# Kernel tuning notes

Hardware: AMD Instinct MI355X
Metric: run time of the kernel (lower is better)

## Reference

```python
import jax, jax.numpy as jnp
import numpy as np

N_NODES = 50000
N_EDGES = 800000
NODE_DIM = 128
EDGE_DIM = 64
HID = 2 * NODE_DIM + EDGE_DIM  # 320


def setup_inputs() -> dict:
    key = jax.random.key(0)
    k1, k2, k3, k4 = jax.random.split(key, 4)
    x = jax.random.normal(k1, (N_NODES, NODE_DIM), dtype=jnp.float32)
    edge_index = jax.random.randint(k2, (2, N_EDGES), 0, N_NODES, dtype=jnp.int32)
    edge_ft = jax.random.normal(k3, (N_EDGES, EDGE_DIM), dtype=jnp.float32)
    kw1, kw2 = jax.random.split(k4)
    scale = 1.0 / np.sqrt(HID)
    W_val = jax.random.uniform(kw1, (NODE_DIM, HID), jnp.float32, -scale, scale)
    b_val = jnp.zeros((NODE_DIM,), jnp.float32)
    W_mul = jax.random.uniform(kw2, (NODE_DIM, HID), jnp.float32, -scale, scale)
    b_mul = jnp.zeros((NODE_DIM,), jnp.float32)
    return {"x": x, "edge_index": edge_index, "edge_ft": edge_ft,
            "W_val": W_val, "b_val": b_val, "W_mul": W_mul, "b_mul": b_mul}


def reference(x, edge_index, edge_ft, W_val, b_val, W_mul, b_mul):
    sender, receiver = edge_index[0], edge_index[1]
    # gather + concat: [E, 2*node_dim + edge_dim]
    c = jnp.concatenate([x[sender], x[receiver], edge_ft], axis=1)
    vals = jax.nn.softplus(c @ W_val.T + b_val)
    gate = jax.nn.sigmoid(c @ W_mul.T + b_mul)
    msg = vals * gate  # [E, node_dim]
    # scatter-sum by receiver into [N, node_dim]
    return jax.ops.segment_sum(msg, receiver, num_segments=x.shape[0])
```

## Files before the change

### kernel.cpp

```cpp
#include <hip/hip_runtime.h>

#define E_EDGES   800000
#define NN_NODES  50000
#define NODE_DIM  128
#define EDGE_DIM  64
#define KDIM      320
#define BM        64
#define BN        64
#define SA        72
#define SM        129
#define SX        136
#define THREADS   512
#define W4UNITS   20480
#define NSCAN     98

typedef _Float16 half8 __attribute__((ext_vector_type(8)));
typedef float    f32x4 __attribute__((ext_vector_type(4)));

__device__ __forceinline__ unsigned short f2h(float f) {
    _Float16 h = (_Float16)f;
    return __builtin_bit_cast(unsigned short, h);
}
__device__ __forceinline__ float h2f(unsigned short u) {
    return (float)__builtin_bit_cast(_Float16, u);
}

__global__ void prep(const float* __restrict__ wv,
                     const float* __restrict__ wm,
                     const int* __restrict__ ei,
                     unsigned short* __restrict__ Wc,
                     unsigned* __restrict__ cnt) {
    int i = blockIdx.x * blockDim.x + threadIdx.x;
    if (i < W4UNITS) {
        const int n4h = (NODE_DIM * KDIM) / 4;
        const float* src = (i < n4h) ? wv : wm;
        int j = (i < n4h) ? i : i - n4h;
        float4 f = ((const float4*)src)[j];
        ushort4 o;
        o.x = f2h(f.x); o.y = f2h(f.y); o.z = f2h(f.z); o.w = f2h(f.w);
        ((ushort4*)Wc)[i] = o;
    } else {
        int e = i - W4UNITS;
        if (e < E_EDGES) atomicAdd(&cnt[ei[E_EDGES + e]], 1u);
    }
}

__global__ void scan1(const unsigned* __restrict__ cnt,
                      unsigned* __restrict__ offs,
                      unsigned* __restrict__ bsum) {
    __shared__ unsigned s[512];
    int tid = threadIdx.x;
    int i = blockIdx.x * 512 + tid;
    unsigned v = (i < NN_NODES) ? cnt[i] : 0u;
    s[tid] = v; __syncthreads();
    for (int off = 1; off < 512; off <<= 1) {
        unsigned t = (tid >= off) ? s[tid - off] : 0u;
        __syncthreads();
        s[tid] += t;
        __syncthreads();
    }
    if (i < NN_NODES) offs[i] = s[tid] - v;
    if (tid == 511) bsum[blockIdx.x] = s[511];
}

__global__ void scan2(unsigned* __restrict__ bsum) {
    __shared__ unsigned s[128];
    int tid = threadIdx.x;
    unsigned v = (tid < NSCAN) ? bsum[tid] : 0u;
    s[tid] = v; __syncthreads();
    for (int off = 1; off < 128; off <<= 1) {
        unsigned t = (tid >= off) ? s[tid - off] : 0u;
        __syncthreads();
        s[tid] += t;
        __syncthreads();
    }
    if (tid < NSCAN) bsum[tid] = s[tid] - v;
}

__global__ void scatter_k(const int* __restrict__ ei,
                          unsigned* __restrict__ offs,
                          const unsigned* __restrict__ bsum,
                          unsigned* __restrict__ perm) {
    int e = blockIdx.x * blockDim.x + threadIdx.x;
    if (e >= E_EDGES) return;
    int r = ei[E_EDGES + e];
    unsigned p = atomicAdd(&offs[r], 1u) + bsum[r >> 9];
    perm[p] = (unsigned)e;
}

__global__ void __launch_bounds__(THREADS, 4)
pcompute(const float* __restrict__ x,
         const unsigned short* __restrict__ Wc,
         const float* __restrict__ bval,
         const float* __restrict__ bmul,
         unsigned short* __restrict__ Ph)
{
    __shared__ unsigned short Xs[BN * SX];
    const int tid  = threadIdx.x;
    const int n0   = blockIdx.x * BN;
    const int lane = tid & 63;
    const int wid  = tid >> 6;
    const int wm   = wid & 1;
    const int wn   = wid >> 1;
    const int q    = lane >> 4;
    const int l16  = lane & 15;

#pragma unroll
    for (int i = 0; i < 2; ++i) {
        int u = tid + i * THREADS;
        int row = u >> 4, seg = u & 15;
        int node = n0 + row;
        if (node >= NN_NODES) node = NN_NODES - 1;
        const float* s = x + (size_t)node * NODE_DIM + seg * 8;
        float4 f0 = ((const float4*)s)[0];
        float4 f1 = ((const float4*)s)[1];
        uint4 v;
        v.x = (unsigned)f2h(f0.x) | ((unsigned)f2h(f0.y) << 16);
        v.y = (unsigned)f2h(f0.z) | ((unsigned)f2h(f0.w) << 16);
        v.z = (unsigned)f2h(f1.x) | ((unsigned)f2h(f1.y) << 16);
        v.w = (unsigned)f2h(f1.z) | ((unsigned)f2h(f1.w) << 16);
        *(uint4*)(&Xs[row * SX + seg * 8]) = v;
    }
    __syncthreads();

#pragma unroll
    for (int nhalf = 0; nhalf < 2; ++nhalf) {
        f32x4 acc[2][4];
        const f32x4 zero4 = {0.f, 0.f, 0.f, 0.f};
#pragma unroll
        for (int mt = 0; mt < 2; ++mt)
#pragma unroll
            for (int nt = 0; nt < 4; ++nt) acc[mt][nt] = zero4;

#pragma unroll
        for (int ks = 0; ks < 4; ++ks) {
            half8 a[2], b[4];
#pragma unroll
            for (int mt = 0; mt < 2; ++mt)
                a[mt] = *(const half8*)(&Xs[(wm * 32 + mt * 16 + l16) * SX + ks * 32 + q * 8]);
#pragma unroll
            for (int nt = 0; nt < 4; ++nt)
                b[nt] = *(const half8*)(Wc + (size_t)(wn * 64 + nt * 16 + l16) * KDIM
                                           + nhalf * 128 + ks * 32 + q * 8);
#pragma unroll
            for (int mt = 0; mt < 2; ++mt)
#pragma unroll
                for (int nt = 0; nt < 4; ++nt)
                    acc[mt][nt] = __builtin_amdgcn_mfma_f32_16x16x32_f16(
                        a[mt], b[nt], acc[mt][nt], 0, 0, 0);
        }

#pragma unroll
        for (int mt = 0; mt < 2; ++mt) {
#pragma unroll
            for (int nt = 0; nt < 4; ++nt) {
                int j  = wn * 64 + nt * 16 + l16;
                int c  = j & 127;
                int vg = j >> 7;
                float bb = 0.f;
                if (nhalf == 0) bb = vg ? bmul[c] : bval[c];
#pragma unroll
                for (int r = 0; r < 4; ++r) {
                    int node = n0 + wm * 32 + mt * 16 + q * 4 + r;
                    if (node < NN_NODES)
                        Ph[(size_t)node * 512 + nhalf * 256 + c * 2 + vg] =
                            f2h(acc[mt][nt][r] + bb);
                }
            }
        }
    }
}

__global__ void __launch_bounds__(THREADS, 4)
cgc_sorted(const unsigned short* __restrict__ Ph,
           const int* __restrict__ ei,
           const float* __restrict__ ef,
           const unsigned short* __restrict__ Wc,
           const unsigned* __restrict__ perm,
           float* __restrict__ out)
{
    __shared__ float msgBuf[BM * SM];
    __shared__ int  eIds[BM];
    __shared__ int  sIdx[BM];
    __shared__ int  rIdx[BM];
    __shared__ int  runStart[BM + 1];
    __shared__ int  slotRecv[BM];
    __shared__ int  nslotsS;

    unsigned short* As = (unsigned short*)msgBuf;

    const int tid  = threadIdx.x;
    const int e0   = blockIdx.x * BM;
    const int lane = tid & 63;
    const int wid  = tid >> 6;
    const int wm   = wid & 1;
    const int wn   = wid >> 1;
    const int q    = lane >> 4;
    const int l16  = lane & 15;

    if (tid < BM) {
        int e = (int)perm[e0 + tid];
        eIds[tid] = e;
        int sN = ei[e];
        int rN = ei[E_EDGES + e];
        sIdx[tid] = sN;
        rIdx[tid] = rN;
        int prev = __shfl_up(rN, 1);
        int flag = (tid == 0) || (prev != rN);
        unsigned long long m = __ballot(flag);
        int slot = __popcll(m & (((unsigned long long)2 << tid) - 1)) - 1;
        if (flag) { runStart[slot] = tid; slotRecv[slot] = rN; }
        if (tid == BM - 1) {
            int ns = (int)__popcll(m);
            nslotsS = ns;
            runStart[ns] = BM;
        }
    }
    __syncthreads();

    {
        int row = tid >> 3, seg = tid & 7;
        const float* s = ef + (size_t)eIds[row] * EDGE_DIM + seg * 8;
        float4 f0 = ((const float4*)s)[0];
        float4 f1 = ((const float4*)s)[1];
        uint4 v;
        v.x = (unsigned)f2h(f0.x) | ((unsigned)f2h(f0.y) << 16);
        v.y = (unsigned)f2h(f0.z) | ((unsigned)f2h(f0.w) << 16);
        v.z = (unsigned)f2h(f1.x) | ((unsigned)f2h(f1.y) << 16);
        v.w = (unsigned)f2h(f1.z) | ((unsigned)f2h(f1.w) << 16);
        *(uint4*)(&As[row * SA + seg * 8]) = v;
    }

    const int nb0 = wn * 32;
    const int nbase[4] = { nb0, nb0 + 16, 128 + nb0, 128 + nb0 + 16 };
    half8 b[2][4];
#pragma unroll
    for (int ks = 0; ks < 2; ++ks)
#pragma unroll
        for (int nt = 0; nt < 4; ++nt)
            b[ks][nt] = *(const half8*)(Wc + (size_t)(nbase[nt] + l16) * KDIM
                                           + 256 + ks * 32 + q * 8);

    f32x4 acc[2][4];
    const f32x4 zero4 = {0.f, 0.f, 0.f, 0.f};
#pragma unroll
    for (int mt = 0; mt < 2; ++mt)
#pragma unroll
        for (int nt = 0; nt < 4; ++nt) acc[mt][nt] = zero4;

    __syncthreads();

#pragma unroll
    for (int ks = 0; ks < 2; ++ks) {
        half8 a[2];
#pragma unroll
        for (int mt = 0; mt < 2; ++mt)
            a[mt] = *(const half8*)(&As[(wm * 32 + mt * 16 + l16) * SA + ks * 32 + q * 8]);
#pragma unroll
        for (int mt = 0; mt < 2; ++mt)
#pragma unroll
            for (int nt = 0; nt < 4; ++nt)
                acc[mt][nt] = __builtin_amdgcn_mfma_f32_16x16x32_f16(
                    a[mt], b[ks][nt], acc[mt][nt], 0, 0, 0);
    }

    __syncthreads();

#pragma unroll
    for (int mt = 0; mt < 2; ++mt) {
#pragma unroll
        for (int r = 0; r < 4; ++r) {
            int row = wm * 32 + mt * 16 + q * 4 + r;
            int sN = sIdx[row];
            int rN = rIdx[row];
            const unsigned* pS = (const unsigned*)(Ph + (size_t)sN * 512);
            const unsigned* pR = (const unsigned*)(Ph + (size_t)rN * 512 + 256);
#pragma unroll
            for (int ct = 0; ct < 2; ++ct) {
                int c = wn * 32 + ct * 16 + l16;
                unsigned us = pS[c];
                unsigned ur = pR[c];
                float v = acc[mt][ct][r]     + h2f((unsigned short)(us & 0xffff))
                                             + h2f((unsigned short)(ur & 0xffff));
                float g = acc[mt][ct + 2][r] + h2f((unsigned short)(us >> 16))
                                             + h2f((unsigned short)(ur >> 16));
                float sp  = fmaxf(v, 0.f) + __logf(1.f + __expf(-fabsf(v)));
                float sig = __builtin_amdgcn_rcpf(1.f + __expf(-g));
                msgBuf[row * SM + c] = sp * sig;
            }
        }
    }
    __syncthreads();

    const int nslots = nslotsS;
    for (int idx = tid; idx < nslots * NODE_DIM; idx += THREADS) {
        int s = idx >> 7, c = idx & 127;
        int rs = runStart[s], re = runStart[s + 1];
        float sum = 0.f;
        for (int row = rs; row < re; ++row) sum += msgBuf[row * SM + c];
        atomicAdd(out + (size_t)slotRecv[s] * NODE_DIM + c, sum);
    }
}

__global__ void __launch_bounds__(THREADS, 4)
cgc_atomic(const unsigned short* __restrict__ Ph,
           const int* __restrict__ ei,
           const float* __restrict__ ef,
           const unsigned short* __restrict__ Wc,
           float* __restrict__ out)
{
    __shared__ unsigned short As[BM * SA];
    __shared__ int sIdx[BM];
    __shared__ int rIdx[BM];

    const int tid  = threadIdx.x;
    const int e0   = blockIdx.x * BM;
    const int lane = tid & 63;
    const int wid  = tid >> 6;
    const int wm   = wid & 1;
    const int wn   = wid >> 1;
    const int q    = lane >> 4;
    const int l16  = lane & 15;

    if (tid < BM) {
        sIdx[tid] = ei[e0 + tid];
        rIdx[tid] = ei[E_EDGES + e0 + tid];
    }
    {
        int row = tid >> 3, seg = tid & 7;
        const float* s = ef + (size_t)(e0 + row) * EDGE_DIM + seg * 8;
        float4 f0 = ((const float4*)s)[0];
        float4 f1 = ((const float4*)s)[1];
        uint4 v;
        v.x = (unsigned)f2h(f0.x) | ((unsigned)f2h(f0.y) << 16);
        v.y = (unsigned)f2h(f0.z) | ((unsigned)f2h(f0.w) << 16);
        v.z = (unsigned)f2h(f1.x) | ((unsigned)f2h(f1.y) << 16);
        v.w = (unsigned)f2h(f1.z) | ((unsigned)f2h(f1.w) << 16);
        *(uint4*)(&As[row * SA + seg * 8]) = v;
    }
    const int nb0 = wn * 32;
    const int nbase[4] = { nb0, nb0 + 16, 128 + nb0, 128 + nb0 + 16 };
    half8 b[2][4];
#pragma unroll
    for (int ks = 0; ks < 2; ++ks)
#pragma unroll
        for (int nt = 0; nt < 4; ++nt)
            b[ks][nt] = *(const half8*)(Wc + (size_t)(nbase[nt] + l16) * KDIM
                                           + 256 + ks * 32 + q * 8);
    f32x4 acc[2][4];
    const f32x4 zero4 = {0.f, 0.f, 0.f, 0.f};
#pragma unroll
    for (int mt = 0; mt < 2; ++mt)
#pragma unroll
        for (int nt = 0; nt < 4; ++nt) acc[mt][nt] = zero4;
    __syncthreads();
#pragma unroll
    for (int ks = 0; ks < 2; ++ks) {
        half8 a[2];
#pragma unroll
        for (int mt = 0; mt < 2; ++mt)
            a[mt] = *(const half8*)(&As[(wm * 32 + mt * 16 + l16) * SA + ks * 32 + q * 8]);
#pragma unroll
        for (int mt = 0; mt < 2; ++mt)
#pragma unroll
            for (int nt = 0; nt < 4; ++nt)
                acc[mt][nt] = __builtin_amdgcn_mfma_f32_16x16x32_f16(
                    a[mt], b[ks][nt], acc[mt][nt], 0, 0, 0);
    }
#pragma unroll
    for (int mt = 0; mt < 2; ++mt) {
#pragma unroll
        for (int r = 0; r < 4; ++r) {
            int row = wm * 32 + mt * 16 + q * 4 + r;
            int sN = sIdx[row];
            int rN = rIdx[row];
            const unsigned* pS = (const unsigned*)(Ph + (size_t)sN * 512);
            const unsigned* pR = (const unsigned*)(Ph + (size_t)rN * 512 + 256);
#pragma unroll
            for (int ct = 0; ct < 2; ++ct) {
                int c = wn * 32 + ct * 16 + l16;
                unsigned us = pS[c];
                unsigned ur = pR[c];
                float v = acc[mt][ct][r]     + h2f((unsigned short)(us & 0xffff))
                                             + h2f((unsigned short)(ur & 0xffff));
                float g = acc[mt][ct + 2][r] + h2f((unsigned short)(us >> 16))
                                             + h2f((unsigned short)(ur >> 16));
                float sp  = fmaxf(v, 0.f) + __logf(1.f + __expf(-fabsf(v)));
                float sig = __builtin_amdgcn_rcpf(1.f + __expf(-g));
                atomicAdd(out + (size_t)rN * NODE_DIM + c, sp * sig);
            }
        }
    }
}


extern "C" void kernel_launch(void* const* d_in, const int* in_sizes, int n_in,
                              void* d_out, int out_size, void* d_ws, size_t ws_size,
                              hipStream_t stream) {
    const float* x  = (const float*)d_in[0];
    const int*   ei = (const int*)d_in[1];
    const float* ef = (const float*)d_in[2];
    const float* Wv = (const float*)d_in[3];
    const float* bv = (const float*)d_in[4];
    const float* Wm = (const float*)d_in[5];
    const float* bm = (const float*)d_in[6];
    float* out = (float*)d_out;

    const size_t oWc   = 0;
    const size_t oPh   = 262144;
    const size_t oCnt  = oPh  + 51200000;
    const size_t oOffs = oCnt + 200704;
    const size_t oBsum = oOffs + 200704;
    const size_t oPerm = oBsum + 512;
    const size_t need_sorted = oPerm + (size_t)E_EDGES * 4;

    unsigned short* Wc = (unsigned short*)((char*)d_ws + oWc);
    unsigned short* Ph = (unsigned short*)((char*)d_ws + oPh);

    hipMemsetAsync(d_out, 0, (size_t)NN_NODES * NODE_DIM * sizeof(float), stream);

    if (ws_size >= need_sorted) {
        unsigned* cnt  = (unsigned*)((char*)d_ws + oCnt);
        unsigned* offs = (unsigned*)((char*)d_ws + oOffs);
        unsigned* bsum = (unsigned*)((char*)d_ws + oBsum);
        unsigned* perm = (unsigned*)((char*)d_ws + oPerm);

        hipMemsetAsync(cnt, 0, NN_NODES * sizeof(unsigned), stream);

        const int totalPrep = W4UNITS + E_EDGES;
        prep<<<(totalPrep + 255) / 256, 256, 0, stream>>>(Wv, Wm, ei, Wc, cnt);
        scan1<<<NSCAN, 512, 0, stream>>>(cnt, offs, bsum);
        scan2<<<1, 128, 0, stream>>>(bsum);
        scatter_k<<<(E_EDGES + 255) / 256, 256, 0, stream>>>(ei, offs, bsum, perm);

        pcompute<<<(NN_NODES + BN - 1) / BN, THREADS, 0, stream>>>(x, Wc, bv, bm, Ph);
        cgc_sorted<<<E_EDGES / BM, THREADS, 0, stream>>>(Ph, ei, ef, Wc, perm, out);
    } else {
        prep<<<(W4UNITS + 255) / 256, 256, 0, stream>>>(Wv, Wm, ei, Wc,
                                                        (unsigned*)((char*)d_ws + oPh));
        pcompute<<<(NN_NODES + BN - 1) / BN, THREADS, 0, stream>>>(x, Wc, bv, bm, Ph);
        cgc_atomic<<<E_EDGES / BM, THREADS, 0, stream>>>(Ph, ei, ef, Wc, out);
    }
}
```

Before: 576.7 us.

## Stage node projections through LDS, swizzle edge tile, use packed fp16 ops

Several micro-optimisations land together. pcompute now writes its fp16 projection rows into a shared-memory tile and stores them to global with coalesced 16-byte writes, replacing scattered 2-byte stores, and its launch bound drops to 2 blocks per CU. The sorted kernel uses an XOR-swizzled LDS layout for the edge-feature tile and a wider msgBuf stride. Conversions switch to packed round-toward-zero cvt_pkrtz, and the sender and receiver projections are summed as half2 before widening. Summing in fp16 and rounding toward zero cost some precision, and the extra LDS tile may lower occupancy of pcompute.

Result: faster. 563.2 us (-2.3%).

```diff
diff --git a/kernel.cpp b/kernel.cpp
--- a/kernel.cpp
+++ b/kernel.cpp
@@ -7,14 +7,18 @@
 #define KDIM      320
 #define BM        64
 #define BN        64
-#define SA        72
-#define SM        129
+#define SWA       64
+#define SM        132
 #define SX        136
+#define SO        264
+#define SAF       72
 #define THREADS   512
 #define W4UNITS   20480
 #define NSCAN     98
 
 typedef _Float16 half8 __attribute__((ext_vector_type(8)));
+typedef _Float16 half2t __attribute__((ext_vector_type(2)));
+typedef __fp16   fp16x2 __attribute__((ext_vector_type(2)));
 typedef float    f32x4 __attribute__((ext_vector_type(4)));
 
 __device__ __forceinline__ unsigned short f2h(float f) {
@@ -23,6 +27,10 @@
 }
 __device__ __forceinline__ float h2f(unsigned short u) {
     return (float)__builtin_bit_cast(_Float16, u);
+}
+__device__ __forceinline__ unsigned pkrtz(float a, float b) {
+    fp16x2 r = __builtin_amdgcn_cvt_pkrtz(a, b);
+    return __builtin_bit_cast(unsigned, r);
 }
 
 __global__ void prep(const float* __restrict__ wv,
@@ -36,9 +44,10 @@
         const float* src = (i < n4h) ? wv : wm;
         int j = (i < n4h) ? i : i - n4h;
         float4 f = ((const float4*)src)[j];
-        ushort4 o;
-        o.x = f2h(f.x); o.y = f2h(f.y); o.z = f2h(f.z); o.w = f2h(f.w);
-        ((ushort4*)Wc)[i] = o;
+        uint2 o;
+        o.x = pkrtz(f.x, f.y);
+        o.y = pkrtz(f.z, f.w);
+        ((uint2*)Wc)[i] = o;
     } else {
         int e = i - W4UNITS;
         if (e < E_EDGES) atomicAdd(&cnt[ei[E_EDGES + e]], 1u);
@@ -88,7 +97,7 @@
     perm[p] = (unsigned)e;
 }
 
-__global__ void __launch_bounds__(THREADS, 4)
+__global__ void __launch_bounds__(THREADS, 2)
 pcompute(const float* __restrict__ x,
          const unsigned short* __restrict__ Wc,
          const float* __restrict__ bval,
@@ -96,6 +105,7 @@
          unsigned short* __restrict__ Ph)
 {
     __shared__ unsigned short Xs[BN * SX];
+    __shared__ unsigned short Os[BN * SO];
     const int tid  = threadIdx.x;
     const int n0   = blockIdx.x * BN;
     const int lane = tid & 63;
@@ -115,10 +125,10 @@
         float4 f0 = ((const float4*)s)[0];
         float4 f1 = ((const float4*)s)[1];
         uint4 v;
-        v.x = (unsigned)f2h(f0.x) | ((unsigned)f2h(f0.y) << 16);
-        v.y = (unsigned)f2h(f0.z) | ((unsigned)f2h(f0.w) << 16);
-        v.z = (unsigned)f2h(f1.x) | ((unsigned)f2h(f1.y) << 16);
-        v.w = (unsigned)f2h(f1.z) | ((unsigned)f2h(f1.w) << 16);
+        v.x = pkrtz(f0.x, f0.y);
+        v.y = pkrtz(f0.z, f0.w);
+        v.z = pkrtz(f1.x, f1.y);
+        v.w = pkrtz(f1.z, f1.w);
         *(uint4*)(&Xs[row * SX + seg * 8]) = v;
     }
     __syncthreads();
@@ -161,13 +171,24 @@
                 if (nhalf == 0) bb = vg ? bmul[c] : bval[c];
 #pragma unroll
                 for (int r = 0; r < 4; ++r) {
-                    int node = n0 + wm * 32 + mt * 16 + q * 4 + r;
-                    if (node < NN_NODES)
-                        Ph[(size_t)node * 512 + nhalf * 256 + c * 2 + vg] =
-                            f2h(acc[mt][nt][r] + bb);
+                    int row = wm * 32 + mt * 16 + q * 4 + r;
+                    Os[row * SO + c * 2 + vg] = f2h(acc[mt][nt][r] + bb);
                 }
             }
         }
+        __syncthreads();
+
+#pragma unroll
+        for (int i = 0; i < 4; ++i) {
+            int u = tid + i * THREADS;
+            int row = u >> 5, seg = u & 31;
+            int node = n0 + row;
+            if (node < NN_NODES) {
+                uint4 v = *(const uint4*)(&Os[row * SO + seg * 8]);
+                *(uint4*)(Ph + (size_t)node * 512 + nhalf * 256 + seg * 8) = v;
+            }
+        }
+        __syncthreads();
     }
 }
 
@@ -224,11 +245,12 @@
         float4 f0 = ((const float4*)s)[0];
         float4 f1 = ((const float4*)s)[1];
         uint4 v;
-        v.x = (unsigned)f2h(f0.x) | ((unsigned)f2h(f0.y) << 16);
-        v.y = (unsigned)f2h(f0.z) | ((unsigned)f2h(f0.w) << 16);
-        v.z = (unsigned)f2h(f1.x) | ((unsigned)f2h(f1.y) << 16);
-        v.w = (unsigned)f2h(f1.z) | ((unsigned)f2h(f1.w) << 16);
-        *(uint4*)(&As[row * SA + seg * 8]) = v;
+        v.x = pkrtz(f0.x, f0.y);
+        v.y = pkrtz(f0.z, f0.w);
+        v.z = pkrtz(f1.x, f1.y);
+        v.w = pkrtz(f1.z, f1.w);
+        int inner = (seg * 8) ^ ((row & 7) << 3);
+        *(uint4*)(&As[row * SWA + inner]) = v;
     }
 
     const int nb0 = wn * 32;
@@ -254,8 +276,11 @@
     for (int ks = 0; ks < 2; ++ks) {
         half8 a[2];
 #pragma unroll
-        for (int mt = 0; mt < 2; ++mt)
-            a[mt] = *(const half8*)(&As[(wm * 32 + mt * 16 + l16) * SA + ks * 32 + q * 8]);
+        for (int mt = 0; mt < 2; ++mt) {
+            int row = wm * 32 + mt * 16 + l16;
+            int inner = (ks * 32 + q * 8) ^ ((row & 7) << 3);
+            a[mt] = *(const half8*)(&As[row * SWA + inner]);
+        }
 #pragma unroll
         for (int mt = 0; mt < 2; ++mt)
 #pragma unroll
@@ -273,17 +298,16 @@
             int row = wm * 32 + mt * 16 + q * 4 + r;
             int sN = sIdx[row];
             int rN = rIdx[row];
-            const unsigned* pS = (const unsigned*)(Ph + (size_t)sN * 512);
-            const unsigned* pR = (const unsigned*)(Ph + (size_t)rN * 512 + 256);
+            const unsigned* pS = (const unsigned*)(Ph + ((size_t)sN << 9));
+            const unsigned* pR = (const unsigned*)(Ph + ((size_t)rN << 9) + 256);
 #pragma unroll
             for (int ct = 0; ct < 2; ++ct) {
                 int c = wn * 32 + ct * 16 + l16;
-                unsigned us = pS[c];
-                unsigned ur = pR[c];
-                float v = acc[mt][ct][r]     + h2f((unsigned short)(us & 0xffff))
-                                             + h2f((unsigned short)(ur & 0xffff));
-                float g = acc[mt][ct + 2][r] + h2f((unsigned short)(us >> 16))
-                                             + h2f((unsigned short)(ur >> 16));
+                half2t hs = __builtin_bit_cast(half2t, pS[c]);
+                half2t hr = __builtin_bit_cast(half2t, pR[c]);
+                half2t t  = hs + hr;
+                float v = acc[mt][ct][r]     + (float)t.x;
+                float g = acc[mt][ct + 2][r] + (float)t.y;
                 float sp  = fmaxf(v, 0.f) + __logf(1.f + __expf(-fabsf(v)));
                 float sig = __builtin_amdgcn_rcpf(1.f + __expf(-g));
                 msgBuf[row * SM + c] = sp * sig;
@@ -297,7 +321,8 @@
         int s = idx >> 7, c = idx & 127;
         int rs = runStart[s], re = runStart[s + 1];
         float sum = 0.f;
-        for (int row = rs; row < re; ++row) sum += msgBuf[row * SM + c];
+        const float* p = &msgBuf[rs * SM + c];
+        for (int row = rs; row < re; ++row) { sum += *p; p += SM; }
         atomicAdd(out + (size_t)slotRecv[s] * NODE_DIM + c, sum);
     }
 }
@@ -309,7 +334,7 @@
            const unsigned short* __restrict__ Wc,
            float* __restrict__ out)
 {
-    __shared__ unsigned short As[BM * SA];
+    __shared__ unsigned short As[BM * SAF];
     __shared__ int sIdx[BM];
     __shared__ int rIdx[BM];
 
@@ -332,11 +357,11 @@
         float4 f0 = ((const float4*)s)[0];
         float4 f1 = ((const float4*)s)[1];
         uint4 v;
-        v.x = (unsigned)f2h(f0.x) | ((unsigned)f2h(f0.y) << 16);
-        v.y = (unsigned)f2h(f0.z) | ((unsigned)f2h(f0.w) << 16);
-        v.z = (unsigned)f2h(f1.x) | ((unsigned)f2h(f1.y) << 16);
-        v.w = (unsigned)f2h(f1.z) | ((unsigned)f2h(f1.w) << 16);
-        *(uint4*)(&As[row * SA + seg * 8]) = v;
+        v.x = pkrtz(f0.x, f0.y);
+        v.y = pkrtz(f0.z, f0.w);
+        v.z = pkrtz(f1.x, f1.y);
+        v.w = pkrtz(f1.z, f1.w);
+        *(uint4*)(&As[row * SAF + seg * 8]) = v;
     }
     const int nb0 = wn * 32;
     const int nbase[4] = { nb0, nb0 + 16, 128 + nb0, 128 + nb0 + 16 };
@@ -359,7 +384,7 @@
         half8 a[2];
 #pragma unroll
         for (int mt = 0; mt < 2; ++mt)
-            a[mt] = *(const half8*)(&As[(wm * 32 + mt * 16 + l16) * SA + ks * 32 + q * 8]);
+            a[mt] = *(const half8*)(&As[(wm * 32 + mt * 16 + l16) * SAF + ks * 32 + q * 8]);
 #pragma unroll
         for (int mt = 0; mt < 2; ++mt)
 #pragma unroll
@@ -374,17 +399,16 @@
             int row = wm * 32 + mt * 16 + q * 4 + r;
             int sN = sIdx[row];
             int rN = rIdx[row];
-            const unsigned* pS = (const unsigned*)(Ph + (size_t)sN * 512);
-            const unsigned* pR = (const unsigned*)(Ph + (size_t)rN * 512 + 256);
+            const unsigned* pS = (const unsigned*)(Ph + ((size_t)sN << 9));
+            const unsigned* pR = (const unsigned*)(Ph + ((size_t)rN << 9) + 256);
 #pragma unroll
             for (int ct = 0; ct < 2; ++ct) {
                 int c = wn * 32 + ct * 16 + l16;
-                unsigned us = pS[c];
-                unsigned ur = pR[c];
-                float v = acc[mt][ct][r]     + h2f((unsigned short)(us & 0xffff))
-                                             + h2f((unsigned short)(ur & 0xffff));
-                float g = acc[mt][ct + 2][r] + h2f((unsigned short)(us >> 16))
-                                             + h2f((unsigned short)(ur >> 16));
+                half2t hs = __builtin_bit_cast(half2t, pS[c]);
+                half2t hr = __builtin_bit_cast(half2t, pR[c]);
+                half2t t  = hs + hr;
+                float v = acc[mt][ct][r]     + (float)t.x;
+                float g = acc[mt][ct + 2][r] + (float)t.y;
                 float sp  = fmaxf(v, 0.f) + __logf(1.f + __expf(-fabsf(v)));
                 float sig = __builtin_amdgcn_rcpf(1.f + __expf(-g));
                 atomicAdd(out + (size_t)rN * NODE_DIM + c, sp * sig);
```
